# Optimization experiments

Measured on AMD Instinct MI355X. Metric: run time of the kernel, lower is better.

The kernel has to match this reference:

```python
import jax, jax.numpy as jnp
import numpy as np

HEADS = 8
DIM_HEAD = 64
DIM = 512
B, N = 4, 2048
SCALE = DIM_HEAD ** -0.5


def setup_inputs() -> dict:
    key = jax.random.key(0)
    k1, k2, k3, k4, k5, k6 = jax.random.split(key, 6)
    inner = HEADS * DIM_HEAD
    s = DIM ** -0.5
    return {
        "input_feature": jax.random.normal(k1, (B, N, DIM), dtype=jnp.float32),
        "mask": jax.random.randint(k2, (B, N), 0, 2, dtype=jnp.int32),
        "Wq": jax.random.normal(k3, (inner, DIM), dtype=jnp.float32) * s,
        "Wk": jax.random.normal(k4, (inner, DIM), dtype=jnp.float32) * s,
        "Wv": jax.random.normal(k5, (inner, DIM), dtype=jnp.float32) * s,
        "Wout": jax.random.normal(k6, (DIM, inner), dtype=jnp.float32) * s,
    }


def reference(input_feature, mask, Wq, Wk, Wv, Wout):
    # Conv1d with kernel_size=1, no bias == per-token linear: out = W @ x_channels
    q = jnp.einsum('bnc,dc->bnd', input_feature, Wq)  # [B, N, H*Dh]
    k = jnp.einsum('bnc,dc->bnd', input_feature, Wk)
    v = jnp.einsum('bnc,dc->bnd', input_feature, Wv)

    # '(n c)' channel layout is head-major -> reshape to [B, N, H, Dh], move head out front
    def split_heads(t):
        return t.reshape(B, N, HEADS, DIM_HEAD).transpose(2, 0, 1, 3)  # [H, B, N, Dh]

    q, k, v = split_heads(q), split_heads(k), split_heads(v)

    scores = jnp.einsum('hbtd,hbsd->hbts', q, k) * SCALE  # [H, B, N, N]
    # masked_fill(mask == 0, 1e-9): fill with small CONSTANT (not -inf), faithful to source
    m = (mask == 0)[None, :, None, :]  # [1, B, 1, N]
    scores = jnp.where(m, jnp.float32(1e-9), scores)
    att = jax.nn.softmax(scores, axis=-1)
    out = jnp.einsum('hbts,hbsd->hbtd', att, v)  # [H, B, N, Dh]

    # '(n b) tokens c -> b (n c) tokens' : head-major channel concat
    out = out.transpose(1, 2, 0, 3).reshape(B, N, HEADS * DIM_HEAD)  # [B, N, H*Dh]
    out = jnp.einsum('bnd,ed->bne', out, Wout)  # [B, N, DIM]
    return out
```

## Files before the change

kernel.cpp:

```cpp
#include <hip/hip_runtime.h>
#include <hip/hip_bf16.h>

typedef __attribute__((ext_vector_type(8))) short short8;
typedef __attribute__((ext_vector_type(4))) short short4_t;
typedef __attribute__((ext_vector_type(4))) float float4_;

#define LOG2E 1.4426950408889634f

__device__ __forceinline__ short f2bf(float f) {
    unsigned int u = __builtin_bit_cast(unsigned int, f);
    u = (u + 0x7FFFu + ((u >> 16) & 1u)) >> 16;
    return (short)u;
}

__device__ __forceinline__ unsigned pk2bf(float a, float b) {
    unsigned ua = __builtin_bit_cast(unsigned, a) + 0x8000u;
    unsigned ub = __builtin_bit_cast(unsigned, b) + 0x8000u;
    return __builtin_amdgcn_perm(ub, ua, 0x07060302);
}

__device__ __forceinline__ void pl32swap(unsigned &a, unsigned &b) {
    auto r = __builtin_amdgcn_permlane32_swap(a, b, false, false);
    a = r[0]; b = r[1];
}
__device__ __forceinline__ void pl16swap(unsigned &a, unsigned &b) {
    auto r = __builtin_amdgcn_permlane16_swap(a, b, false, false);
    a = r[0]; b = r[1];
}

union U4 { unsigned u[4]; short8 s; };

__device__ __forceinline__ void gload_lds16(const short* g, short* l) {
    __builtin_amdgcn_global_load_lds((const __attribute__((address_space(1))) void*)g,
                                     (__attribute__((address_space(3))) void*)l, 16, 0, 0);
}

__global__ __launch_bounds__(256) void cvt_kernel(
    const float* __restrict__ X, const float* __restrict__ Wq, const float* __restrict__ Wk,
    const float* __restrict__ Wv, const float* __restrict__ Wo,
    short* __restrict__ Xb, short* __restrict__ Wqkvb, short* __restrict__ Wob) {
    int i = blockIdx.x * 256 + threadIdx.x;
    const float* src; short* dst; float sc = 1.0f;
    if (i < 1048576) { src = X + (size_t)i * 4; dst = Xb + (size_t)i * 4; }
    else {
        int w = i - 1048576; int sec = w >> 16; int j = (w & 65535) * 4;
        if (sec == 0)      { src = Wq + j; dst = Wqkvb + j; sc = 0.125f * LOG2E; }
        else if (sec == 1) { src = Wk + j; dst = Wqkvb + 262144 + j; }
        else if (sec == 2) { src = Wv + j; dst = Wqkvb + 524288 + j; }
        else               { src = Wo + j; dst = Wob + j; }
    }
    float4 v = *(const float4*)src;
    short4_t o;
    o[0] = f2bf(v.x * sc); o[1] = f2bf(v.y * sc); o[2] = f2bf(v.z * sc); o[3] = f2bf(v.w * sc);
    *(short4_t*)dst = o;
}

__global__ __launch_bounds__(256) void gemm_qkv(const short* __restrict__ A, const short* __restrict__ B,
                                                const int* __restrict__ mask,
                                                short* __restrict__ Qb, short* __restrict__ Kb,
                                                short* __restrict__ Vtb) {
    __shared__ __align__(16) short smemAB[2 * 8192];
    __shared__ int maskL[128];
    short* At = smemAB;
    short* Bt = smemAB + 8192;
    constexpr int K = 512;
    int tid = threadIdx.x;
    int wid = tid >> 6, lane = tid & 63;
    int quad = lane >> 4, cc = lane & 15;
    int c7 = cc & 7;
    int wr = wid >> 1, wc = wid & 1;
    int m0 = blockIdx.y * 128, n0 = blockIdx.x * 128;
    if (tid < 128) maskL[tid] = mask[m0 + tid];

    const short* gA[4]; const short* gB[4]; int lofs[4];
#pragma unroll
    for (int p = 0; p < 4; ++p) {
        int slot = p * 256 + tid;
        int r = slot >> 3, c = slot & 7;
        int cs = (c ^ (r & 7)) * 8;
        gA[p] = A + (size_t)(m0 + r) * K + cs;
        gB[p] = B + (size_t)(n0 + r) * K + cs;
        lofs[p] = slot * 8;
    }
    short8 arg[4], brg[4];
#pragma unroll
    for (int p = 0; p < 4; ++p) { arg[p] = *(const short8*)gA[p]; brg[p] = *(const short8*)gB[p]; }

    float4_ acc[4][4] = {};

    for (int kk = 0; kk < K; kk += 64) {
        __syncthreads();
#pragma unroll
        for (int p = 0; p < 4; ++p) {
            *(short8*)(At + lofs[p]) = arg[p];
            *(short8*)(Bt + lofs[p]) = brg[p];
        }
        if (kk < K - 64) {
#pragma unroll
            for (int p = 0; p < 4; ++p) {
                arg[p] = *(const short8*)(gA[p] + kk + 64);
                brg[p] = *(const short8*)(gB[p] + kk + 64);
            }
        }
        __syncthreads();
#pragma unroll
        for (int kc = 0; kc < 2; ++kc) {
            short8 af[4], bf[4];
#pragma unroll
            for (int i = 0; i < 4; ++i)
                af[i] = *(const short8*)(At + (wr * 64 + i * 16 + cc) * 64 + (((kc * 4 + quad) ^ c7) * 8));
#pragma unroll
            for (int j = 0; j < 4; ++j)
                bf[j] = *(const short8*)(Bt + (wc * 64 + j * 16 + cc) * 64 + (((kc * 4 + quad) ^ c7) * 8));
#pragma unroll
            for (int i = 0; i < 4; ++i)
#pragma unroll
                for (int j = 0; j < 4; ++j)
                    acc[i][j] = __builtin_amdgcn_mfma_f32_16x16x32_bf16(af[i], bf[j], acc[i][j], 0, 0, 0);
        }
    }

    int which = n0 >> 9;
    int b = m0 >> 11;
    if (which == 2) {
        __syncthreads();
        short* T = smemAB;
#pragma unroll
        for (int i = 0; i < 4; ++i) {
#pragma unroll
            for (int j = 0; j < 4; ++j) {
                int d_l = wc * 64 + j * 16 + cc;
                int nnb = wr * 64 + i * 16 + quad * 4;
                int G = nnb >> 3, half = (nnb >> 2) & 1;
                int Gs = G ^ (d_l & 15);
                short4_t pv;
                pv[0] = f2bf(acc[i][j][0]); pv[1] = f2bf(acc[i][j][1]);
                pv[2] = f2bf(acc[i][j][2]); pv[3] = f2bf(acc[i][j][3]);
                *(short4_t*)(T + d_l * 128 + Gs * 8 + half * 4) = pv;
            }
        }
        __syncthreads();
#pragma unroll
        for (int p = 0; p < 8; ++p) {
            int slot = p * 256 + tid;
            int d = slot >> 4, G = slot & 15;
            short8 v = *(const short8*)(T + d * 128 + ((G ^ (d & 15)) * 8));
            *(short8*)(Vtb + ((size_t)(b * 512 + (n0 & 511) + d)) * 2048 + (m0 & 2047) + G * 8) = v;
        }
    } else {
        short* dst = which ? Kb : Qb;
#pragma unroll
        for (int i = 0; i < 4; ++i) {
#pragma unroll
            for (int j = 0; j < 4; ++j) {
#pragma unroll
                for (int r = 0; r < 4; ++r) {
                    int lm = wr * 64 + i * 16 + quad * 4 + r;
                    int nn = (m0 & 2047) + lm;
                    int hd = (n0 & 511) + wc * 64 + j * 16 + cc;
                    int h = hd >> 6, dh = hd & 63;
                    float v = acc[i][j][r];
                    if (which == 1 && maskL[lm] == 0) v = 0.0f;
                    dst[((((size_t)b * 8 + h) * 2048 + nn) * 64) + dh] = f2bf(v);
                }
            }
        }
    }
}

__global__ __launch_bounds__(256, 4) void attn_kernel(const short* __restrict__ Q, const short* __restrict__ Kg,
                                                      const short* __restrict__ Vt,
                                                      short* __restrict__ AO) {
    __shared__ __align__(16) short KbufL[2 * 4096];
    __shared__ __align__(16) short VbufL[2 * 4096];

    int tid = threadIdx.x;
    int w = tid >> 6, lane = tid & 63;
    int quad = lane >> 4, cc = lane & 15;
    int c7 = cc & 7;
    int bh = blockIdx.x, b = bh >> 3, h = bh & 7;
    int t0 = blockIdx.y * 64 + w * 16;
    size_t kbase = (size_t)bh * 2048 * 64;
    size_t vbase = (size_t)b * 512 * 2048 + (size_t)h * 64 * 2048;

    short8 qf[2];
#pragma unroll
    for (int kc = 0; kc < 2; ++kc)
        qf[kc] = *(const short8*)(Q + kbase + (size_t)(t0 + cc) * 64 + kc * 32 + quad * 8);

    int koff[4][2];
#pragma unroll
    for (int rb = 0; rb < 4; ++rb)
#pragma unroll
        for (int kc = 0; kc < 2; ++kc)
            koff[rb][kc] = (rb * 16 + cc) * 64 + (((kc * 4 + quad) ^ c7) * 8);

    int sA = tid >> 3, cA = tid & 7;
    const short* gK0 = Kg + kbase + (size_t)sA * 64 + ((cA ^ (sA & 7)) * 8);
    const short* gK1 = gK0 + 32 * 64;
    const short* gV0 = Vt + vbase + (size_t)sA * 2048 + ((cA ^ (sA & 7)) * 8);
    const short* gV1 = gV0 + 32 * 2048;
    int ld0 = tid * 8, ld1 = tid * 8 + 2048;

    short8 krg0 = *(const short8*)gK0, krg1 = *(const short8*)gK1;
    short8 vrg0 = *(const short8*)gV0, vrg1 = *(const short8*)gV1;
    gK0 += 4096; gK1 += 4096; gV0 += 64; gV1 += 64;
    *(short8*)(KbufL + ld0) = krg0; *(short8*)(KbufL + ld1) = krg1;
    *(short8*)(VbufL + ld0) = vrg0; *(short8*)(VbufL + ld1) = vrg1;
    krg0 = *(const short8*)gK0; krg1 = *(const short8*)gK1;
    vrg0 = *(const short8*)gV0; vrg1 = *(const short8*)gV1;
    gK0 += 4096; gK1 += 4096; gV0 += 64; gV1 += 64;

    float4_ o[4] = {};
    float lp = 0.f;

#pragma unroll 2
    for (int it = 0; it < 32; ++it) {
        __syncthreads();
        int cur = it & 1;
        const short* Kt  = KbufL + cur * 4096;
        const short* Vtt = VbufL + cur * 4096;
        if (it < 31) {
            short* Kn = KbufL + (cur ^ 1) * 4096;
            short* Vn = VbufL + (cur ^ 1) * 4096;
            *(short8*)(Kn + ld0) = krg0; *(short8*)(Kn + ld1) = krg1;
            *(short8*)(Vn + ld0) = vrg0; *(short8*)(Vn + ld1) = vrg1;
        }
        if (it < 30) {
            krg0 = *(const short8*)gK0; krg1 = *(const short8*)gK1;
            vrg0 = *(const short8*)gV0; vrg1 = *(const short8*)gV1;
            gK0 += 4096; gK1 += 4096; gV0 += 64; gV1 += 64;
        }

        float4_ acc[4];
        __builtin_amdgcn_s_setprio(1);
#pragma unroll
        for (int sb = 0; sb < 4; ++sb) {
            short8 kf0 = *(const short8*)(Kt + koff[sb][0]);
            short8 kf1 = *(const short8*)(Kt + koff[sb][1]);
            float4_ z = {0.f, 0.f, 0.f, 0.f};
            z = __builtin_amdgcn_mfma_f32_16x16x32_bf16(kf0, qf[0], z, 0, 0, 0);
            acc[sb] = __builtin_amdgcn_mfma_f32_16x16x32_bf16(kf1, qf[1], z, 0, 0, 0);
        }
        __builtin_amdgcn_s_setprio(0);

        unsigned Wp[4][2];
#pragma unroll
        for (int sb = 0; sb < 4; ++sb) {
            float x0 = __builtin_amdgcn_exp2f(acc[sb][0]);
            float x1 = __builtin_amdgcn_exp2f(acc[sb][1]);
            float x2 = __builtin_amdgcn_exp2f(acc[sb][2]);
            float x3 = __builtin_amdgcn_exp2f(acc[sb][3]);
            lp += (x0 + x1) + (x2 + x3);
            Wp[sb][0] = pk2bf(x0, x1);
            Wp[sb][1] = pk2bf(x2, x3);
        }

        short8 pa[2];
#pragma unroll
        for (int kc = 0; kc < 2; ++kc) {
            unsigned a0 = Wp[2 * kc][0], a1 = Wp[2 * kc][1];
            unsigned b0 = Wp[2 * kc + 1][0], b1 = Wp[2 * kc + 1][1];
            pl32swap(a0, b0); pl32swap(a1, b1);
            pl16swap(a0, b0); pl16swap(a1, b1);
            U4 u; u.u[0] = a0; u.u[1] = a1; u.u[2] = b0; u.u[3] = b1;
            pa[kc] = u.s;
        }

        __builtin_amdgcn_s_setprio(1);
#pragma unroll
        for (int db = 0; db < 4; ++db) {
            short8 vf0 = *(const short8*)(Vtt + koff[db][0]);
            short8 vf1 = *(const short8*)(Vtt + koff[db][1]);
            o[db] = __builtin_amdgcn_mfma_f32_16x16x32_bf16(pa[0], vf0, o[db], 0, 0, 0);
            o[db] = __builtin_amdgcn_mfma_f32_16x16x32_bf16(pa[1], vf1, o[db], 0, 0, 0);
        }
        __builtin_amdgcn_s_setprio(0);
    }

    float s = lp;
    s += __shfl_xor(s, 16, 64);
    s += __shfl_xor(s, 32, 64);
    float inv = 1.0f / s;
#pragma unroll
    for (int r = 0; r < 4; ++r) {
        int tl = quad * 4 + r;
        float iv = __shfl(inv, tl, 64);
        size_t rowbase = ((size_t)(b * 2048 + t0 + tl)) * 512 + h * 64;
#pragma unroll
        for (int db = 0; db < 4; ++db)
            AO[rowbase + db * 16 + cc] = f2bf(o[db][r] * iv);
    }
}

__global__ __launch_bounds__(256) void gemm_out(const short* __restrict__ A, const short* __restrict__ B,
                                                float* __restrict__ C) {
    __shared__ short At[64 * 64];
    __shared__ short Bt[64 * 64];
    constexpr int K = 512;
    int tid = threadIdx.x;
    int wid = tid >> 6, lane = tid & 63;
    int quad = lane >> 4, cc = lane & 15;
    int c7 = cc & 7;
    int wr = wid >> 1, wc = wid & 1;
    int m0 = blockIdx.y * 64, n0 = blockIdx.x * 64;

    float4_ acc[2][2] = {};

    for (int kk = 0; kk < K; kk += 64) {
#pragma unroll
        for (int p = 0; p < 2; ++p) {
            int slot = p * 256 + tid;
            int r = slot >> 3, c = slot & 7;
            int cs = (c ^ (r & 7)) * 8;
            gload_lds16(A + (size_t)(m0 + r) * K + kk + cs, At + slot * 8);
            gload_lds16(B + (size_t)(n0 + r) * K + kk + cs, Bt + slot * 8);
        }
        __syncthreads();
#pragma unroll
        for (int kc = 0; kc < 2; ++kc) {
            short8 af[2], bf[2];
#pragma unroll
            for (int i = 0; i < 2; ++i)
                af[i] = *(const short8*)(At + (wr * 32 + i * 16 + cc) * 64 + (((kc * 4 + quad) ^ c7) * 8));
#pragma unroll
            for (int j = 0; j < 2; ++j)
                bf[j] = *(const short8*)(Bt + (wc * 32 + j * 16 + cc) * 64 + (((kc * 4 + quad) ^ c7) * 8));
#pragma unroll
            for (int i = 0; i < 2; ++i)
#pragma unroll
                for (int j = 0; j < 2; ++j)
                    acc[i][j] = __builtin_amdgcn_mfma_f32_16x16x32_bf16(af[i], bf[j], acc[i][j], 0, 0, 0);
        }
        __syncthreads();
    }

#pragma unroll
    for (int i = 0; i < 2; ++i)
#pragma unroll
        for (int j = 0; j < 2; ++j)
#pragma unroll
            for (int r = 0; r < 4; ++r) {
                int gm = m0 + wr * 32 + i * 16 + quad * 4 + r;
                int gn = n0 + wc * 32 + j * 16 + cc;
                C[(size_t)gm * 512 + gn] = acc[i][j][r];
            }
}

extern "C" void kernel_launch(void* const* d_in, const int* in_sizes, int n_in,
                              void* d_out, int out_size, void* d_ws, size_t ws_size,
                              hipStream_t stream) {
    const float* X  = (const float*)d_in[0];
    const int* mask = (const int*)d_in[1];
    const float* Wq = (const float*)d_in[2];
    const float* Wk = (const float*)d_in[3];
    const float* Wv = (const float*)d_in[4];
    const float* Wo = (const float*)d_in[5];

    char* ws = (char*)d_ws;
    short* Xbf   = (short*)(ws + 0);
    short* Wqkvb = (short*)(ws + 8388608);
    short* Wob   = (short*)(ws + 9961472);
    short* Qb    = (short*)(ws + 10485760);
    short* Kb    = (short*)(ws + 18874368);
    short* Vtb   = (short*)(ws + 27262976);
    short* AOb   = (short*)(ws + 35651584);

    cvt_kernel<<<5120, 256, 0, stream>>>(X, Wq, Wk, Wv, Wo, Xbf, Wqkvb, Wob);
    gemm_qkv<<<dim3(12, 64), 256, 0, stream>>>(Xbf, Wqkvb, mask, Qb, Kb, Vtb);
    attn_kernel<<<dim3(32, 32), 256, 0, stream>>>(Qb, Kb, Vtb, AOb);
    gemm_out<<<dim3(8, 128), 256, 0, stream>>>(AOb, Wob, (float*)d_out);
}
```

Measured before the change: 164.2 us.

## Enlarge gemm_out M tile and prefetch next K slice through registers

The output projection GEMM now computes a 128x64 tile per block instead of 64x64, halving the grid and doubling A-operand reuse per B load. The direct global-to-LDS loads are replaced with register-staged prefetch: the next K slice is loaded into registers while the current slice is computed, then written to shared memory after a barrier. This aims to hide global load latency and cut per-block overhead, at the cost of more registers and fewer blocks (512) for occupancy.

```diff
diff --git a/kernel.cpp b/kernel.cpp
--- a/kernel.cpp
+++ b/kernel.cpp
@@ -295,53 +295,79 @@
 
 __global__ __launch_bounds__(256) void gemm_out(const short* __restrict__ A, const short* __restrict__ B,
                                                 float* __restrict__ C) {
-    __shared__ short At[64 * 64];
-    __shared__ short Bt[64 * 64];
+    __shared__ __align__(16) short smemAB[8192 + 4096];
+    short* At = smemAB;
+    short* Bt = smemAB + 8192;
     constexpr int K = 512;
     int tid = threadIdx.x;
     int wid = tid >> 6, lane = tid & 63;
     int quad = lane >> 4, cc = lane & 15;
     int c7 = cc & 7;
     int wr = wid >> 1, wc = wid & 1;
-    int m0 = blockIdx.y * 64, n0 = blockIdx.x * 64;
-
-    float4_ acc[2][2] = {};
+    int m0 = blockIdx.y * 128, n0 = blockIdx.x * 64;
+
+    const short* gA[4]; const short* gB[2]; int lofsA[4], lofsB[2];
+#pragma unroll
+    for (int p = 0; p < 4; ++p) {
+        int slot = p * 256 + tid;
+        int r = slot >> 3, c = slot & 7;
+        int cs = (c ^ (r & 7)) * 8;
+        gA[p] = A + (size_t)(m0 + r) * K + cs;
+        lofsA[p] = slot * 8;
+    }
+#pragma unroll
+    for (int p = 0; p < 2; ++p) {
+        int slot = p * 256 + tid;
+        int r = slot >> 3, c = slot & 7;
+        int cs = (c ^ (r & 7)) * 8;
+        gB[p] = B + (size_t)(n0 + r) * K + cs;
+        lofsB[p] = slot * 8;
+    }
+    short8 arg[4], brg[2];
+#pragma unroll
+    for (int p = 0; p < 4; ++p) arg[p] = *(const short8*)gA[p];
+#pragma unroll
+    for (int p = 0; p < 2; ++p) brg[p] = *(const short8*)gB[p];
+
+    float4_ acc[4][2] = {};
 
     for (int kk = 0; kk < K; kk += 64) {
-#pragma unroll
-        for (int p = 0; p < 2; ++p) {
-            int slot = p * 256 + tid;
-            int r = slot >> 3, c = slot & 7;
-            int cs = (c ^ (r & 7)) * 8;
-            gload_lds16(A + (size_t)(m0 + r) * K + kk + cs, At + slot * 8);
-            gload_lds16(B + (size_t)(n0 + r) * K + kk + cs, Bt + slot * 8);
+        __syncthreads();
+#pragma unroll
+        for (int p = 0; p < 4; ++p) *(short8*)(At + lofsA[p]) = arg[p];
+#pragma unroll
+        for (int p = 0; p < 2; ++p) *(short8*)(Bt + lofsB[p]) = brg[p];
+        if (kk < K - 64) {
+#pragma unroll
+            for (int p = 0; p < 4; ++p) arg[p] = *(const short8*)(gA[p] + kk + 64);
+#pragma unroll
+            for (int p = 0; p < 2; ++p) brg[p] = *(const short8*)(gB[p] + kk + 64);
         }
         __syncthreads();
 #pragma unroll
         for (int kc = 0; kc < 2; ++kc) {
-            short8 af[2], bf[2];
-#pragma unroll
-            for (int i = 0; i < 2; ++i)
-                af[i] = *(const short8*)(At + (wr * 32 + i * 16 + cc) * 64 + (((kc * 4 + quad) ^ c7) * 8));
+            short8 af[4], bf[2];
+#pragma unroll
+            for (int i = 0; i < 4; ++i)
+                af[i] = *(const short8*)(At + (wr * 64 + i * 16 + cc) * 64 + (((kc * 4 + quad) ^ c7) * 8));
 #pragma unroll
             for (int j = 0; j < 2; ++j)
                 bf[j] = *(const short8*)(Bt + (wc * 32 + j * 16 + cc) * 64 + (((kc * 4 + quad) ^ c7) * 8));
 #pragma unroll
-            for (int i = 0; i < 2; ++i)
+            for (int i = 0; i < 4; ++i)
 #pragma unroll
                 for (int j = 0; j < 2; ++j)
                     acc[i][j] = __builtin_amdgcn_mfma_f32_16x16x32_bf16(af[i], bf[j], acc[i][j], 0, 0, 0);
         }
-        __syncthreads();
-    }
-
-#pragma unroll
-    for (int i = 0; i < 2; ++i)
+    }
+
+#pragma unroll
+    for (int i = 0; i < 4; ++i)
 #pragma unroll
         for (int j = 0; j < 2; ++j)
 #pragma unroll
             for (int r = 0; r < 4; ++r) {
-                int gm = m0 + wr * 32 + i * 16 + quad * 4 + r;
+                int gm = m0 + wr * 64 + i * 16 + quad * 4 + r;
                 int gn = n0 + wc * 32 + j * 16 + cc;
                 C[(size_t)gm * 512 + gn] = acc[i][j][r];
             }
@@ -369,5 +395,5 @@
     cvt_kernel<<<5120, 256, 0, stream>>>(X, Wq, Wk, Wv, Wo, Xbf, Wqkvb, Wob);
     gemm_qkv<<<dim3(12, 64), 256, 0, stream>>>(Xbf, Wqkvb, mask, Qb, Kb, Vtb);
     attn_kernel<<<dim3(32, 32), 256, 0, stream>>>(Qb, Kb, Vtb, AOb);
-    gemm_out<<<dim3(8, 128), 256, 0, stream>>>(AOb, Wob, (float*)d_out);
-}
+    gemm_out<<<dim3(8, 64), 256, 0, stream>>>(AOb, Wob, (float*)d_out);
+}
```

Result: no change. 164.5 us, median of 2 (+0.2%).
